# Optimization experiments

Measured on AMD Instinct MI355X. Metric: run time of the kernel, lower is better.

Reference implementation:

```python
import jax, jax.numpy as jnp
import numpy as np

DIM = 256
NUM_HEADS = 8
AGENT_NUM = 49
POOL = 7  # int(sqrt(agent_num))


def setup_inputs() -> dict:
    key = jax.random.key(0)
    k1, k2, k3, k4, k5 = jax.random.split(key, 5)
    x = jax.random.normal(k1, (8, 8, 8, 14, 14, DIM), dtype=jnp.float32)
    wq = jax.random.normal(k2, (DIM, DIM), dtype=jnp.float32) * 0.02
    wkv = jax.random.normal(k3, (2 * DIM, DIM), dtype=jnp.float32) * 0.02
    w_proj = jax.random.normal(k4, (DIM, DIM), dtype=jnp.float32) * 0.02
    b_proj = jax.random.normal(k5, (DIM,), dtype=jnp.float32) * 0.02
    return {"x": x, "wq": wq, "wkv": wkv, "w_proj": w_proj, "b_proj": b_proj}


def reference(x, wq, wkv, w_proj, b_proj):
    B, Hh, Ww, wh, ww, c = x.shape
    b = B * Hh * Ww
    n = wh * ww
    H, W = ww, wh  # module uses (H, W) = (window_width, window_height)
    nh = NUM_HEADS
    hd = c // nh
    scale = hd ** -0.5

    xt = x.reshape(b, n, c)  # (b x y)(w1 w2) d
    q = xt @ wq.T                          # [b, n, c]
    kv = xt @ wkv.T                        # [b, n, 2c]
    k, v = kv[..., :c], kv[..., c:]

    # agent tokens: adaptive avg pool q over the window grid to POOL x POOL
    qs = q.reshape(b, H, W, c)
    agent = qs.reshape(b, POOL, H // POOL, POOL, W // POOL, c).mean(axis=(2, 4))
    agent = agent.reshape(b, AGENT_NUM, c)

    # split heads -> [b, nh, seq, hd]
    qh = q.reshape(b, n, nh, hd).transpose(0, 2, 1, 3)
    kh = k.reshape(b, n, nh, hd).transpose(0, 2, 1, 3)
    vh = v.reshape(b, n, nh, hd).transpose(0, 2, 1, 3)
    ah = agent.reshape(b, AGENT_NUM, nh, hd).transpose(0, 2, 1, 3)

    # stage 1: agents attend over k/v
    agent_attn = jax.nn.softmax(jnp.einsum('bhad,bhnd->bhan', ah * scale, kh), axis=-1)
    agent_v = jnp.einsum('bhan,bhnd->bhad', agent_attn, vh)

    # stage 2: queries attend over agents
    q_attn = jax.nn.softmax(jnp.einsum('bhnd,bhad->bhna', qh * scale, ah), axis=-1)
    out = jnp.einsum('bhna,bhad->bhnd', q_attn, agent_v)

    out = out.transpose(0, 2, 1, 3).reshape(b, n, c)
    out = out @ w_proj.T + b_proj
    # rearrange '(b x y) (i j) c -> b x y i j c' with i = window_width
    return out.reshape(B, Hh, Ww, ww, wh, c)
```

## Files before the change

kernel.cpp:

```cpp
#include <hip/hip_runtime.h>

typedef unsigned short u16;
typedef __attribute__((ext_vector_type(8))) short bf16x8;
typedef __attribute__((ext_vector_type(4))) float f32x4;

#define M_ROWS 100352
#define NB     512
#define NTOK   196
#define CDIM   256
#define NHEADS 8
#define HDIM   32
#define ANUM   49
#define PLSTRIDE 6272

__device__ __forceinline__ u16 f2bf(float f) {
    union { float f; unsigned u; } c; c.f = f;
    return (u16)((c.u + 0x7FFFu + ((c.u >> 16) & 1u)) >> 16);
}
__device__ __forceinline__ float bf2f(u16 u) {
    union { unsigned u; float f; } c; c.u = ((unsigned)u) << 16;
    return c.f;
}

#define NX4 6422528
__global__ __launch_bounds__(256)
void cast_all(const float* __restrict__ x, const float* __restrict__ wq,
              const float* __restrict__ wkv, const float* __restrict__ wproj,
              u16* __restrict__ xb, u16* __restrict__ wqkvb,
              u16* __restrict__ wprojb)
{
    const int idx4 = blockIdx.x * 256 + threadIdx.x;
    const float* src; u16* dst; int off;
    if (idx4 < NX4)               { src = x;     dst = xb;             off = idx4; }
    else if (idx4 < NX4 + 16384)  { src = wq;    dst = wqkvb;          off = idx4 - NX4; }
    else if (idx4 < NX4 + 49152)  { src = wkv;   dst = wqkvb + 65536;  off = idx4 - NX4 - 16384; }
    else                          { src = wproj; dst = wprojb;         off = idx4 - NX4 - 49152; }
    float4 v = *reinterpret_cast<const float4*>(&src[(size_t)off * 4]);
    ushort4 o;
    o.x = f2bf(v.x); o.y = f2bf(v.y); o.z = f2bf(v.z); o.w = f2bf(v.w);
    *reinterpret_cast<ushort4*>(&dst[(size_t)off * 4]) = o;
}

#define GLD 40
__global__ __launch_bounds__(256)
void gemm_qkv(const u16* __restrict__ xb, const u16* __restrict__ wqkvb,
              u16* __restrict__ qh, u16* __restrict__ kh, u16* __restrict__ vh)
{
    __shared__ u16 As[128 * GLD];
    __shared__ u16 Bs[128 * GLD];

    const int tid  = threadIdx.x;
    const int lane = tid & 63, wid = tid >> 6;
    const int wm = wid >> 1, wn = wid & 1;
    const int row0 = blockIdx.x * 128;
    const int col0 = blockIdx.y * 128;

    f32x4 acc[4][4] = {};
    const int lrow = lane & 15;
    const int lk   = (lane >> 4) * 8;

    for (int k0 = 0; k0 < 256; k0 += 32) {
        #pragma unroll
        for (int i = 0; i < 2; ++i) {
            const int c = tid + i * 256;
            const int r = c >> 2, kc = c & 3;
            bf16x8 va = *reinterpret_cast<const bf16x8*>(
                &xb[(size_t)(row0 + r) * 256 + k0 + kc * 8]);
            *reinterpret_cast<bf16x8*>(&As[r * GLD + kc * 8]) = va;
            bf16x8 vb = *reinterpret_cast<const bf16x8*>(
                &wqkvb[(size_t)(col0 + r) * 256 + k0 + kc * 8]);
            *reinterpret_cast<bf16x8*>(&Bs[r * GLD + kc * 8]) = vb;
        }
        __syncthreads();

        bf16x8 af[4], bfr[4];
        #pragma unroll
        for (int m = 0; m < 4; ++m)
            af[m] = *reinterpret_cast<bf16x8*>(&As[(wm*64 + m*16 + lrow) * GLD + lk]);
        #pragma unroll
        for (int n = 0; n < 4; ++n)
            bfr[n] = *reinterpret_cast<bf16x8*>(&Bs[(wn*64 + n*16 + lrow) * GLD + lk]);
        #pragma unroll
        for (int m = 0; m < 4; ++m)
            #pragma unroll
            for (int n = 0; n < 4; ++n)
                acc[m][n] = __builtin_amdgcn_mfma_f32_16x16x32_bf16(
                                af[m], bfr[n], acc[m][n], 0, 0, 0);
        __syncthreads();
    }

    #pragma unroll
    for (int n = 0; n < 4; ++n) {
        const int ccol = col0 + wn*64 + n*16 + (lane & 15);
        const int pl = ccol >> 8;
        const int hh = (ccol >> 5) & 7;
        const int d  = ccol & 31;
        u16* base = (pl == 0) ? qh : (pl == 1) ? kh : vh;
        #pragma unroll
        for (int m = 0; m < 4; ++m) {
            const int rbase = row0 + wm*64 + m*16 + (lane >> 4) * 4;
            #pragma unroll
            for (int r = 0; r < 4; ++r) {
                const unsigned row = rbase + r;
                const unsigned bb = row / 196u;
                const unsigned nn = row - bb * 196u;
                base[((size_t)(bb*8 + hh) * 196 + nn) * 32 + d] = f2bf(acc[m][n][r]);
            }
        }
    }
}

__global__ __launch_bounds__(256)
void gemm_proj(const u16* __restrict__ qh, const u16* __restrict__ Bw,
               const float* __restrict__ bias, float* __restrict__ C)
{
    __shared__ u16 As[128 * GLD];
    __shared__ u16 Bs[128 * GLD];

    const int tid  = threadIdx.x;
    const int lane = tid & 63, wid = tid >> 6;
    const int wm = wid >> 1, wn = wid & 1;
    const int row0 = blockIdx.x * 128;
    const int col0 = blockIdx.y * 128;

    f32x4 acc[4][4] = {};
    const int lrow = lane & 15;
    const int lk   = (lane >> 4) * 8;

    for (int k0 = 0; k0 < 256; k0 += 32) {
        const int hh = k0 >> 5;
        #pragma unroll
        for (int i = 0; i < 2; ++i) {
            const int c = tid + i * 256;
            const int r = c >> 2, kc = c & 3;
            const unsigned row = row0 + r;
            const unsigned bb = row / 196u;
            const unsigned nn = row - bb * 196u;
            bf16x8 va = *reinterpret_cast<const bf16x8*>(
                &qh[((size_t)(bb*8 + hh) * 196 + nn) * 32 + kc * 8]);
            *reinterpret_cast<bf16x8*>(&As[r * GLD + kc * 8]) = va;
            bf16x8 vb = *reinterpret_cast<const bf16x8*>(
                &Bw[(size_t)(col0 + r) * 256 + k0 + kc * 8]);
            *reinterpret_cast<bf16x8*>(&Bs[r * GLD + kc * 8]) = vb;
        }
        __syncthreads();

        bf16x8 af[4], bfr[4];
        #pragma unroll
        for (int m = 0; m < 4; ++m)
            af[m] = *reinterpret_cast<bf16x8*>(&As[(wm*64 + m*16 + lrow) * GLD + lk]);
        #pragma unroll
        for (int n = 0; n < 4; ++n)
            bfr[n] = *reinterpret_cast<bf16x8*>(&Bs[(wn*64 + n*16 + lrow) * GLD + lk]);
        #pragma unroll
        for (int m = 0; m < 4; ++m)
            #pragma unroll
            for (int n = 0; n < 4; ++n)
                acc[m][n] = __builtin_amdgcn_mfma_f32_16x16x32_bf16(
                                af[m], bfr[n], acc[m][n], 0, 0, 0);
        __syncthreads();
    }

    #pragma unroll
    for (int n = 0; n < 4; ++n) {
        const int ccol = col0 + wn*64 + n*16 + (lane & 15);
        const float bv = bias[ccol];
        #pragma unroll
        for (int m = 0; m < 4; ++m) {
            const int rbase = row0 + wm*64 + m*16 + (lane >> 4) * 4;
            #pragma unroll
            for (int r = 0; r < 4; ++r)
                C[(size_t)(rbase + r) * 256 + ccol] = acc[m][n][r] + bv;
        }
    }
}

#define SA_LD   40
#define SVT_LD  232
#define SP1_LD  232
#define SAVT_LD 72
#define SP2_LD  72
#define OFF_A   0
#define OFF_VT  2560
#define OFF_P1  9984
#define OFF_AVT 24832
#define OFF_P2  2560
#define LDS_U16 27136

__global__ __launch_bounds__(256, 3)
void fused_attn(const u16* __restrict__ kh, const u16* __restrict__ vh,
                u16* __restrict__ qh)
{
    __shared__ __align__(16) u16 lds[LDS_U16];
    const int tid  = threadIdx.x;
    const int lane = tid & 63, w = tid >> 6;
    const int li = lane & 15, g = lane >> 4;
    const int bh = blockIdx.x;
    const float scale = 0.1767766952966369f;
    const f32x4 z = {0.f, 0.f, 0.f, 0.f};
    const bf16x8 zv = {0,0,0,0,0,0,0,0};
    const ushort4 z4 = {0,0,0,0};

    const u16* ksl = kh + (size_t)bh * PLSTRIDE;
    const u16* vsl = vh + (size_t)bh * PLSTRIDE;
    u16*       qsl = qh + (size_t)bh * PLSTRIDE;

    for (int i = tid; i < 60; i += 256) {
        const int row = 49 + (i >> 2), kc = i & 3;
        *reinterpret_cast<bf16x8*>(&lds[OFF_A + row * SA_LD + kc * 8]) = zv;
    }
    for (int i = tid; i < 224; i += 256) {
        const int row = i / 7, c4 = 196 + (i % 7) * 4;
        *reinterpret_cast<ushort4*>(&lds[OFF_VT + row * SVT_LD + c4]) = z4;
    }
    for (int i = tid; i < 128; i += 256) {
        const int row = i >> 1, c = 208 + (i & 1) * 8;
        *reinterpret_cast<bf16x8*>(&lds[OFF_P1 + row * SP1_LD + c]) = zv;
    }

    for (int i = tid; i < ANUM * 8; i += 256) {
        const int a = i >> 3, dq = (i & 7) * 4;
        const int p1 = a / 7, p2 = a - p1 * 7;
        float s0 = 0.f, s1 = 0.f, s2 = 0.f, s3 = 0.f;
        #pragma unroll
        for (int i2 = 0; i2 < 2; ++i2)
            #pragma unroll
            for (int j2 = 0; j2 < 2; ++j2) {
                const int n = (p1*2 + i2) * 14 + p2*2 + j2;
                ushort4 v = *reinterpret_cast<const ushort4*>(&qsl[n * 32 + dq]);
                s0 += bf2f(v.x); s1 += bf2f(v.y);
                s2 += bf2f(v.z); s3 += bf2f(v.w);
            }
        const float cc = 0.25f * scale;
        ushort4 o;
        o.x = f2bf(s0 * cc); o.y = f2bf(s1 * cc);
        o.z = f2bf(s2 * cc); o.w = f2bf(s3 * cc);
        *reinterpret_cast<ushort4*>(&lds[OFF_A + a * SA_LD + dq]) = o;
    }

    for (int i = tid; i < NTOK * 4; i += 256) {
        const int n = i >> 2, dc = i & 3;
        bf16x8 v = *reinterpret_cast<const bf16x8*>(&vsl[i * 8]);
        #pragma unroll
        for (int j2 = 0; j2 < 8; ++j2)
            lds[OFF_VT + (dc * 8 + j2) * SVT_LD + n] = (u16)v[j2];
    }
    __syncthreads();

    {
        bf16x8 af = *reinterpret_cast<bf16x8*>(&lds[OFF_A + (w*16 + li) * SA_LD + g*8]);
        f32x4 c[13];
        #pragma unroll
        for (int j = 0; j < 13; ++j) {
            int krow = j*16 + li; krow = krow > 195 ? 195 : krow;
            bf16x8 kf = *reinterpret_cast<const bf16x8*>(&ksl[krow * 32 + g*8]);
            c[j] = __builtin_amdgcn_mfma_f32_16x16x32_bf16(af, kf, z, 0, 0, 0);
        }
        #pragma unroll
        for (int r = 0; r < 4; ++r) {
            float m = -1e30f;
            #pragma unroll
            for (int j = 0; j < 13; ++j)
                if (j < 12 || li < 4) m = fmaxf(m, c[j][r]);
            #pragma unroll
            for (int d = 1; d < 16; d <<= 1) m = fmaxf(m, __shfl_xor(m, d));
            float p[13]; float su = 0.f;
            #pragma unroll
            for (int j = 0; j < 13; ++j) {
                p[j] = (j < 12 || li < 4) ? __expf(c[j][r] - m) : 0.f;
                su += p[j];
            }
            #pragma unroll
            for (int d = 1; d < 16; d <<= 1) su += __shfl_xor(su, d);
            const float inv = 1.f / su;
            const int arow = w*16 + g*4 + r;
            #pragma unroll
            for (int j = 0; j < 13; ++j)
                lds[OFF_P1 + arow * SP1_LD + j*16 + li] = f2bf(p[j] * inv);
        }
    }
    __syncthreads();

    #pragma unroll
    for (int dt = 0; dt < 2; ++dt) {
        f32x4 acc = z;
        #pragma unroll
        for (int kk = 0; kk < 7; ++kk) {
            bf16x8 pa = *reinterpret_cast<bf16x8*>(
                &lds[OFF_P1 + (w*16 + li) * SP1_LD + kk*32 + g*8]);
            bf16x8 vb = *reinterpret_cast<bf16x8*>(
                &lds[OFF_VT + (dt*16 + li) * SVT_LD + kk*32 + g*8]);
            acc = __builtin_amdgcn_mfma_f32_16x16x32_bf16(pa, vb, acc, 0, 0, 0);
        }
        #pragma unroll
        for (int r = 0; r < 4; ++r)
            lds[OFF_AVT + (dt*16 + li) * SAVT_LD + w*16 + g*4 + r] = f2bf(acc[r]);
    }
    __syncthreads();

    {
        bf16x8 ab[4];
        #pragma unroll
        for (int at = 0; at < 4; ++at)
            ab[at] = *reinterpret_cast<bf16x8*>(&lds[OFF_A + (at*16 + li) * SA_LD + g*8]);
        for (int j = w; j < 13; j += 4) {
            const int qrow = min(j*16 + li, NTOK - 1);
            bf16x8 qf = *reinterpret_cast<const bf16x8*>(&qsl[qrow * 32 + g*8]);
            f32x4 cc[4];
            #pragma unroll
            for (int at = 0; at < 4; ++at)
                cc[at] = __builtin_amdgcn_mfma_f32_16x16x32_bf16(qf, ab[at], z, 0, 0, 0);
            #pragma unroll
            for (int r = 0; r < 4; ++r) {
                float m = -1e30f;
                #pragma unroll
                for (int at = 0; at < 4; ++at)
                    if (at < 3 || li < 1) m = fmaxf(m, cc[at][r]);
                #pragma unroll
                for (int d = 1; d < 16; d <<= 1) m = fmaxf(m, __shfl_xor(m, d));
                float p[4]; float su = 0.f;
                #pragma unroll
                for (int at = 0; at < 4; ++at) {
                    p[at] = (at < 3 || li < 1) ? __expf(cc[at][r] - m) : 0.f;
                    su += p[at];
                }
                #pragma unroll
                for (int d = 1; d < 16; d <<= 1) su += __shfl_xor(su, d);
                const float inv = 1.f / su;
                const int trow = j*16 + g*4 + r;
                #pragma unroll
                for (int at = 0; at < 4; ++at)
                    lds[OFF_P2 + trow * SP2_LD + at*16 + li] = f2bf(p[at] * inv);
            }
        }
    }
    __syncthreads();

    for (int j = w; j < 13; j += 4) {
        #pragma unroll
        for (int dt = 0; dt < 2; ++dt) {
            f32x4 acc = z;
            #pragma unroll
            for (int kk = 0; kk < 2; ++kk) {
                bf16x8 pf = *reinterpret_cast<bf16x8*>(
                    &lds[OFF_P2 + (j*16 + li) * SP2_LD + kk*32 + g*8]);
                bf16x8 avf = *reinterpret_cast<bf16x8*>(
                    &lds[OFF_AVT + (dt*16 + li) * SAVT_LD + kk*32 + g*8]);
                acc = __builtin_amdgcn_mfma_f32_16x16x32_bf16(pf, avf, acc, 0, 0, 0);
            }
            #pragma unroll
            for (int r = 0; r < 4; ++r) {
                const int t = j*16 + g*4 + r;
                if (t < NTOK)
                    qsl[t * 32 + dt*16 + li] = f2bf(acc[r]);
            }
        }
    }
}

extern "C" void kernel_launch(void* const* d_in, const int* in_sizes, int n_in,
                              void* d_out, int out_size, void* d_ws, size_t ws_size,
                              hipStream_t stream)
{
    const float* x     = (const float*)d_in[0];
    const float* wq    = (const float*)d_in[1];
    const float* wkv   = (const float*)d_in[2];
    const float* wproj = (const float*)d_in[3];
    const float* bproj = (const float*)d_in[4];
    float* out = (float*)d_out;

    u16* wqkvb  = (u16*)d_ws;
    u16* wprojb = wqkvb  + 196608;
    u16* xb     = wprojb + 65536;
    u16* qh     = xb     + (size_t)M_ROWS * CDIM;
    u16* kh     = qh     + (size_t)M_ROWS * CDIM;
    u16* vh     = kh     + (size_t)M_ROWS * CDIM;

    const dim3 blk(256);

    cast_all<<<dim3(25344), blk, 0, stream>>>(x, wq, wkv, wproj, xb, wqkvb, wprojb);
    gemm_qkv<<<dim3(M_ROWS/128, 6), blk, 0, stream>>>(xb, wqkvb, qh, kh, vh);
    fused_attn<<<dim3(NB*NHEADS), blk, 0, stream>>>(kh, vh, qh);
    gemm_proj<<<dim3(M_ROWS/128, 2), blk, 0, stream>>>(qh, wprojb, bproj, out);
}
```

Baseline: 403.2 us.

## Use direct global-to-LDS loads in GEMMs and transpose softmax MFMA layout

The QKV and projection GEMMs now stage tiles with global_load_lds 16-byte direct loads into unpadded LDS buffers. This bypasses the register round trip, at the risk of LDS bank conflicts now that the padding is gone. In the attention kernel the score MFMAs swap operands so each lane holds one row's scores across its registers. Softmax reductions then need only two cross-lane shuffles instead of four per row, and the probabilities are written as packed 8-byte stores instead of scalar bf16 stores.

```diff
diff --git a/kernel.cpp b/kernel.cpp
--- a/kernel.cpp
+++ b/kernel.cpp
@@ -20,6 +20,14 @@
 __device__ __forceinline__ float bf2f(u16 u) {
     union { unsigned u; float f; } c; c.u = ((unsigned)u) << 16;
     return c.f;
+}
+__device__ __forceinline__ unsigned pack2(float a, float b) {
+    return (unsigned)f2bf(a) | ((unsigned)f2bf(b) << 16);
+}
+__device__ __forceinline__ void gload16(const void* g, void* l) {
+    __builtin_amdgcn_global_load_lds(
+        (const __attribute__((address_space(1))) void*)g,
+        (__attribute__((address_space(3))) void*)l, 16, 0, 0);
 }
 
 #define NX4 6422528
@@ -41,13 +49,12 @@
     *reinterpret_cast<ushort4*>(&dst[(size_t)off * 4]) = o;
 }
 
-#define GLD 40
 __global__ __launch_bounds__(256)
 void gemm_qkv(const u16* __restrict__ xb, const u16* __restrict__ wqkvb,
               u16* __restrict__ qh, u16* __restrict__ kh, u16* __restrict__ vh)
 {
-    __shared__ u16 As[128 * GLD];
-    __shared__ u16 Bs[128 * GLD];
+    __shared__ __align__(16) u16 As[128 * 32];
+    __shared__ __align__(16) u16 Bs[128 * 32];
 
     const int tid  = threadIdx.x;
     const int lane = tid & 63, wid = tid >> 6;
@@ -60,26 +67,20 @@
     const int lk   = (lane >> 4) * 8;
 
     for (int k0 = 0; k0 < 256; k0 += 32) {
-        #pragma unroll
-        for (int i = 0; i < 2; ++i) {
-            const int c = tid + i * 256;
-            const int r = c >> 2, kc = c & 3;
-            bf16x8 va = *reinterpret_cast<const bf16x8*>(
-                &xb[(size_t)(row0 + r) * 256 + k0 + kc * 8]);
-            *reinterpret_cast<bf16x8*>(&As[r * GLD + kc * 8]) = va;
-            bf16x8 vb = *reinterpret_cast<const bf16x8*>(
-                &wqkvb[(size_t)(col0 + r) * 256 + k0 + kc * 8]);
-            *reinterpret_cast<bf16x8*>(&Bs[r * GLD + kc * 8]) = vb;
+        for (int c = wid; c < 8; c += 4) {
+            const int r = c * 16 + (lane >> 2), q = lane & 3;
+            gload16(&xb[(size_t)(row0 + r) * 256 + k0 + q * 8], &As[c * 512]);
+            gload16(&wqkvb[(size_t)(col0 + r) * 256 + k0 + q * 8], &Bs[c * 512]);
         }
         __syncthreads();
 
         bf16x8 af[4], bfr[4];
         #pragma unroll
         for (int m = 0; m < 4; ++m)
-            af[m] = *reinterpret_cast<bf16x8*>(&As[(wm*64 + m*16 + lrow) * GLD + lk]);
+            af[m] = *reinterpret_cast<bf16x8*>(&As[(wm*64 + m*16 + lrow) * 32 + lk]);
         #pragma unroll
         for (int n = 0; n < 4; ++n)
-            bfr[n] = *reinterpret_cast<bf16x8*>(&Bs[(wn*64 + n*16 + lrow) * GLD + lk]);
+            bfr[n] = *reinterpret_cast<bf16x8*>(&Bs[(wn*64 + n*16 + lrow) * 32 + lk]);
         #pragma unroll
         for (int m = 0; m < 4; ++m)
             #pragma unroll
@@ -114,8 +115,8 @@
 void gemm_proj(const u16* __restrict__ qh, const u16* __restrict__ Bw,
                const float* __restrict__ bias, float* __restrict__ C)
 {
-    __shared__ u16 As[128 * GLD];
-    __shared__ u16 Bs[128 * GLD];
+    __shared__ __align__(16) u16 As[128 * 32];
+    __shared__ __align__(16) u16 Bs[128 * 32];
 
     const int tid  = threadIdx.x;
     const int lane = tid & 63, wid = tid >> 6;
@@ -129,29 +130,23 @@
 
     for (int k0 = 0; k0 < 256; k0 += 32) {
         const int hh = k0 >> 5;
-        #pragma unroll
-        for (int i = 0; i < 2; ++i) {
-            const int c = tid + i * 256;
-            const int r = c >> 2, kc = c & 3;
+        for (int c = wid; c < 8; c += 4) {
+            const int r = c * 16 + (lane >> 2), q = lane & 3;
             const unsigned row = row0 + r;
             const unsigned bb = row / 196u;
             const unsigned nn = row - bb * 196u;
-            bf16x8 va = *reinterpret_cast<const bf16x8*>(
-                &qh[((size_t)(bb*8 + hh) * 196 + nn) * 32 + kc * 8]);
-            *reinterpret_cast<bf16x8*>(&As[r * GLD + kc * 8]) = va;
-            bf16x8 vb = *reinterpret_cast<const bf16x8*>(
-                &Bw[(size_t)(col0 + r) * 256 + k0 + kc * 8]);
-            *reinterpret_cast<bf16x8*>(&Bs[r * GLD + kc * 8]) = vb;
+            gload16(&qh[((size_t)(bb*8 + hh) * 196 + nn) * 32 + q * 8], &As[c * 512]);
+            gload16(&Bw[(size_t)(col0 + r) * 256 + k0 + q * 8], &Bs[c * 512]);
         }
         __syncthreads();
 
         bf16x8 af[4], bfr[4];
         #pragma unroll
         for (int m = 0; m < 4; ++m)
-            af[m] = *reinterpret_cast<bf16x8*>(&As[(wm*64 + m*16 + lrow) * GLD + lk]);
+            af[m] = *reinterpret_cast<bf16x8*>(&As[(wm*64 + m*16 + lrow) * 32 + lk]);
         #pragma unroll
         for (int n = 0; n < 4; ++n)
-            bfr[n] = *reinterpret_cast<bf16x8*>(&Bs[(wn*64 + n*16 + lrow) * GLD + lk]);
+            bfr[n] = *reinterpret_cast<bf16x8*>(&Bs[(wn*64 + n*16 + lrow) * 32 + lk]);
         #pragma unroll
         for (int m = 0; m < 4; ++m)
             #pragma unroll
@@ -254,29 +249,34 @@
         for (int j = 0; j < 13; ++j) {
             int krow = j*16 + li; krow = krow > 195 ? 195 : krow;
             bf16x8 kf = *reinterpret_cast<const bf16x8*>(&ksl[krow * 32 + g*8]);
-            c[j] = __builtin_amdgcn_mfma_f32_16x16x32_bf16(af, kf, z, 0, 0, 0);
-        }
-        #pragma unroll
-        for (int r = 0; r < 4; ++r) {
-            float m = -1e30f;
-            #pragma unroll
-            for (int j = 0; j < 13; ++j)
-                if (j < 12 || li < 4) m = fmaxf(m, c[j][r]);
-            #pragma unroll
-            for (int d = 1; d < 16; d <<= 1) m = fmaxf(m, __shfl_xor(m, d));
-            float p[13]; float su = 0.f;
-            #pragma unroll
-            for (int j = 0; j < 13; ++j) {
-                p[j] = (j < 12 || li < 4) ? __expf(c[j][r] - m) : 0.f;
-                su += p[j];
-            }
-            #pragma unroll
-            for (int d = 1; d < 16; d <<= 1) su += __shfl_xor(su, d);
-            const float inv = 1.f / su;
-            const int arow = w*16 + g*4 + r;
-            #pragma unroll
-            for (int j = 0; j < 13; ++j)
-                lds[OFF_P1 + arow * SP1_LD + j*16 + li] = f2bf(p[j] * inv);
+            c[j] = __builtin_amdgcn_mfma_f32_16x16x32_bf16(kf, af, z, 0, 0, 0);
+        }
+        float m = -1e30f;
+        #pragma unroll
+        for (int j = 0; j < 13; ++j)
+            #pragma unroll
+            for (int r = 0; r < 4; ++r)
+                m = (j < 12 || g == 0) ? fmaxf(m, c[j][r]) : m;
+        m = fmaxf(m, __shfl_xor(m, 16));
+        m = fmaxf(m, __shfl_xor(m, 32));
+        float su = 0.f;
+        #pragma unroll
+        for (int j = 0; j < 13; ++j)
+            #pragma unroll
+            for (int r = 0; r < 4; ++r) {
+                const float p = (j < 12 || g == 0) ? __expf(c[j][r] - m) : 0.f;
+                c[j][r] = p; su += p;
+            }
+        su += __shfl_xor(su, 16);
+        su += __shfl_xor(su, 32);
+        const float inv = 1.f / su;
+        const int pbase = OFF_P1 + (w*16 + li) * SP1_LD + g*4;
+        #pragma unroll
+        for (int j = 0; j < 13; ++j) {
+            uint2 pk;
+            pk.x = pack2(c[j][0] * inv, c[j][1] * inv);
+            pk.y = pack2(c[j][2] * inv, c[j][3] * inv);
+            *reinterpret_cast<uint2*>(&lds[pbase + j*16]) = pk;
         }
     }
     __syncthreads();
@@ -292,9 +292,11 @@
                 &lds[OFF_VT + (dt*16 + li) * SVT_LD + kk*32 + g*8]);
             acc = __builtin_amdgcn_mfma_f32_16x16x32_bf16(pa, vb, acc, 0, 0, 0);
         }
-        #pragma unroll
-        for (int r = 0; r < 4; ++r)
-            lds[OFF_AVT + (dt*16 + li) * SAVT_LD + w*16 + g*4 + r] = f2bf(acc[r]);
+        uint2 pk;
+        pk.x = pack2(acc[0], acc[1]);
+        pk.y = pack2(acc[2], acc[3]);
+        *reinterpret_cast<uint2*>(
+            &lds[OFF_AVT + (dt*16 + li) * SAVT_LD + w*16 + g*4]) = pk;
     }
     __syncthreads();
 
@@ -309,28 +311,36 @@
             f32x4 cc[4];
             #pragma unroll
             for (int at = 0; at < 4; ++at)
-                cc[at] = __builtin_amdgcn_mfma_f32_16x16x32_bf16(qf, ab[at], z, 0, 0, 0);
-            #pragma unroll
-            for (int r = 0; r < 4; ++r) {
-                float m = -1e30f;
+                cc[at] = __builtin_amdgcn_mfma_f32_16x16x32_bf16(ab[at], qf, z, 0, 0, 0);
+            float m = -1e30f;
+            #pragma unroll
+            for (int at = 0; at < 4; ++at)
                 #pragma unroll
-                for (int at = 0; at < 4; ++at)
-                    if (at < 3 || li < 1) m = fmaxf(m, cc[at][r]);
+                for (int r = 0; r < 4; ++r)
+                    m = (at < 3 || (g == 0 && r == 0)) ? fmaxf(m, cc[at][r]) : m;
+            m = fmaxf(m, __shfl_xor(m, 16));
+            m = fmaxf(m, __shfl_xor(m, 32));
+            float su = 0.f;
+            #pragma unroll
+            for (int at = 0; at < 4; ++at)
                 #pragma unroll
-                for (int d = 1; d < 16; d <<= 1) m = fmaxf(m, __shfl_xor(m, d));
-                float p[4]; float su = 0.f;
+                for (int r = 0; r < 4; ++r) {
+                    const float p = (at < 3 || (g == 0 && r == 0))
+                                        ? __expf(cc[at][r] - m) : 0.f;
+                    cc[at][r] = p; su += p;
+                }
+            su += __shfl_xor(su, 16);
+            su += __shfl_xor(su, 32);
+            const float inv = 1.f / su;
+            if (j < 12 || li < 4) {
+                const int pbase = OFF_P2 + (j*16 + li) * SP2_LD + g*4;
                 #pragma unroll
                 for (int at = 0; at < 4; ++at) {
-                    p[at] = (at < 3 || li < 1) ? __expf(cc[at][r] - m) : 0.f;
-                    su += p[at];
+                    uint2 pk;
+                    pk.x = pack2(cc[at][0] * inv, cc[at][1] * inv);
+                    pk.y = pack2(cc[at][2] * inv, cc[at][3] * inv);
+                    *reinterpret_cast<uint2*>(&lds[pbase + at*16]) = pk;
                 }
-                #pragma unroll
-                for (int d = 1; d < 16; d <<= 1) su += __shfl_xor(su, d);
-                const float inv = 1.f / su;
-                const int trow = j*16 + g*4 + r;
-                #pragma unroll
-                for (int at = 0; at < 4; ++at)
-                    lds[OFF_P2 + trow * SP2_LD + at*16 + li] = f2bf(p[at] * inv);
             }
         }
     }
```

Measured after the change: 385.7 us. 1.05x faster.
